# Performance work log

Measured on AMD Instinct MI355X. Metric: run time of the kernel, lower is better.

## Reference

```python
import jax, jax.numpy as jnp
import numpy as np

B, S, D, H = 4, 2048, 512, 8
HD = D // H


def rotate_half(t):
    half = t.shape[-1] // 2
    return jnp.concatenate([-t[..., half:], t[..., :half]], axis=-1)


def setup_inputs() -> dict:
    key = jax.random.key(0)
    ks = jax.random.split(key, 8)
    x = jax.random.normal(ks[0], (B, S, D), dtype=jnp.float32)
    # realistic rotary tables built from angles
    inv_freq = 1.0 / (10000.0 ** (jnp.arange(0, D // 2, dtype=jnp.float32) / (D // 2)))
    ang = jnp.arange(S, dtype=jnp.float32)[:, None] * inv_freq[None, :]  # [S, D/2]
    ang = jnp.concatenate([ang, ang], axis=-1)  # [S, D]
    cos_emb = jnp.cos(ang)[None]  # [1, S, D]
    sin_emb = jnp.sin(ang)[None]
    mask = jax.random.randint(ks[1], (B, S, S), 0, 2).astype(jnp.bool_)
    scale = 1.0 / np.sqrt(D)
    wq = jax.random.normal(ks[2], (D, D), dtype=jnp.float32) * scale
    wk = jax.random.normal(ks[3], (D, D), dtype=jnp.float32) * scale
    wv = jax.random.normal(ks[4], (D, D), dtype=jnp.float32) * scale
    wo = jax.random.normal(ks[5], (D, D), dtype=jnp.float32) * scale
    return {"x": x, "cos_emb": cos_emb, "sin_emb": sin_emb, "mask": mask,
            "wq": wq, "wk": wk, "wv": wv, "wo": wo}


def reference(x, cos_emb, sin_emb, mask, wq, wk, wv, wo):
    bsz, seqlen, dim = x.shape
    # projections (weights stored as [in, out])
    xq = x @ wq
    xk = x @ wk
    xv = x @ wv
    # RoPE applied over full dim before head split (as in original)
    xq = xq * cos_emb + rotate_half(xq) * sin_emb
    xk = xk * cos_emb + rotate_half(xk) * sin_emb
    # split heads: [B, H, S, HD]
    xq = xq.reshape(bsz, seqlen, H, HD).transpose(0, 2, 1, 3)
    xk = xk.reshape(bsz, seqlen, H, HD).transpose(0, 2, 1, 3)
    xv = xv.reshape(bsz, seqlen, H, HD).transpose(0, 2, 1, 3)
    scores = jnp.einsum('bhqd,bhkd->bhqk', xq, xk) / jnp.sqrt(jnp.float32(HD))
    scores = scores + (~mask)[:, None].astype(scores.dtype) * (-1e9)
    scores = jax.nn.softmax(scores.astype(jnp.float32), axis=-1).astype(xq.dtype)
    scores = scores * mask[:, None].astype(scores.dtype)
    out = jnp.einsum('bhqk,bhkd->bhqd', scores, xv)
    out = out.transpose(0, 2, 1, 3).reshape(bsz, seqlen, dim)
    return out @ wo
```

## Files before the change

kernel.cpp:

```cpp
#include <hip/hip_runtime.h>
#include <hip/hip_bf16.h>

typedef __bf16 bf16x8 __attribute__((ext_vector_type(8)));
typedef float f32x4 __attribute__((ext_vector_type(4)));
typedef short short8 __attribute__((ext_vector_type(8)));

#define MFMA16(a, b, c) __builtin_amdgcn_mfma_f32_16x16x32_bf16((a), (b), (c), 0, 0, 0)

static constexpr int S = 2048;
static constexpr int D = 512;
static constexpr int HD = 64;
static constexpr int KBLK = 64;
#define QSCALE 0.18033688011112042f

typedef __attribute__((address_space(1))) const unsigned int gu32;
typedef __attribute__((address_space(3))) unsigned int lu32;

__device__ __forceinline__ void gll16(const void* g, void* l) {
  __builtin_amdgcn_global_load_lds((gu32*)g, (lu32*)l, 16, 0, 0);
}

__device__ __forceinline__ unsigned short f2b(float f) {
  return __builtin_bit_cast(unsigned short, __float2bfloat16(f));
}
__device__ __forceinline__ float b2f(unsigned short u) {
  return __builtin_bit_cast(float, (unsigned)u << 16);
}

__global__ void prep_kernel(const float* __restrict__ x, unsigned short* __restrict__ xb,
                            const int* __restrict__ m, unsigned long long* __restrict__ bits,
                            const float* __restrict__ wq, const float* __restrict__ wk,
                            const float* __restrict__ wv, const float* __restrict__ wo,
                            unsigned short* __restrict__ wqkvT, unsigned short* __restrict__ woT) {
  __shared__ float t[64][65];
  const int blk = blockIdx.x;
  const int tid = threadIdx.x;
  if (blk < 4096) {
    int idx = blk * 256 + tid;
    float4 v = ((const float4*)x)[idx];
    ushort4 o;
    o.x = f2b(v.x); o.y = f2b(v.y); o.z = f2b(v.z); o.w = f2b(v.w);
    ((ushort4*)xb)[idx] = o;
  } else if (blk < 6144) {
    const int stride = 2048 * 256;
    const int lane0 = (tid & 63) == 0;
    for (int gid = (blk - 4096) * 256 + tid; gid < 4 * 2048 * 2048; gid += stride) {
      unsigned long long w = __ballot(m[gid] != 0);
      if (lane0) bits[gid >> 6] = w;
    }
  } else {
    const int tt = blk - 6144;
    const int z = tt >> 6, r = tt & 63;
    const float* w = (z == 0) ? wq : (z == 1) ? wk : (z == 2) ? wv : wo;
    unsigned short* dst = (z < 3) ? wqkvT + (size_t)z * 512 * 512 : woT;
    const int i0 = (r & 7) * 64, o0 = (r >> 3) * 64;
    for (int it = 0; it < 16; ++it) {
      int idx = it * 256 + tid;
      int ii = idx >> 6, oo = idx & 63;
      t[oo][ii] = w[(size_t)(i0 + ii) * 512 + o0 + oo];
    }
    __syncthreads();
    for (int it = 0; it < 16; ++it) {
      int idx = it * 256 + tid;
      int oo = idx >> 6, ii = idx & 63;
      int o = o0 + oo, od;
      if (z < 2) {
        const int hh = o >> 6, ff = (o >> 5) & 1, cc = o & 31;
        od = ((hh & 3) * 2 + ff) * 64 + ((hh >> 2) << 5) + cc;
      } else {
        od = o;
      }
      dst[(size_t)od * 512 + i0 + ii] = f2b(t[oo][ii]);
    }
  }
}

__global__ __launch_bounds__(256)
void gemm2(const unsigned short* __restrict__ A, const unsigned short* __restrict__ Bt,
           const float* __restrict__ cose, const float* __restrict__ sine,
           unsigned short* __restrict__ qd, unsigned short* __restrict__ kd,
           unsigned short* __restrict__ vtd) {
  __shared__ alignas(16) unsigned char smem[36864];
  unsigned short (*lds)[2][4096] = (unsigned short (*)[2][4096])smem;
  const int tid = threadIdx.x;
  const int lane = tid & 63, l15 = lane & 15, lg = lane >> 4;
  const int wave = tid >> 6;
  const int K = 512;
  const int m0 = blockIdx.x * 128, n0 = blockIdx.y * 128;
  const int wm = (wave >> 1) * 64, wn = (wave & 1) * 64;
  const int wbase = wave * 512;
  const int grow = tid >> 2, gcol = (tid & 3) * 8;
  f32x4 acc[4][4] = {};

#define GSTAGE(sb, kk)                                                              \
  do {                                                                              \
    gll16(&A[(size_t)(m0 + grow) * K + (kk) + gcol], &lds[sb][0][wbase]);           \
    gll16(&A[(size_t)(m0 + 64 + grow) * K + (kk) + gcol], &lds[sb][0][2048 + wbase]);\
    gll16(&Bt[(size_t)(n0 + grow) * K + (kk) + gcol], &lds[sb][1][wbase]);          \
    gll16(&Bt[(size_t)(n0 + 64 + grow) * K + (kk) + gcol], &lds[sb][1][2048 + wbase]);\
  } while (0)

  GSTAGE(0, 0);
  asm volatile("s_waitcnt vmcnt(0)" ::: "memory");
  __syncthreads();
  for (int t = 0; t < 16; ++t) {
    const int cur = t & 1;
    if (t + 1 < 16) GSTAGE(cur ^ 1, (t + 1) * 32);
    bf16x8 af[4], bfr[4];
#pragma unroll
    for (int i = 0; i < 4; ++i) {
      af[i]  = *(const bf16x8*)&lds[cur][0][(wm + i * 16 + l15) * 32 + lg * 8];
      bfr[i] = *(const bf16x8*)&lds[cur][1][(wn + i * 16 + l15) * 32 + lg * 8];
    }
    __builtin_amdgcn_s_setprio(1);
#pragma unroll
    for (int i = 0; i < 4; ++i)
#pragma unroll
      for (int j = 0; j < 4; ++j)
        acc[i][j] = MFMA16(af[i], bfr[j], acc[i][j]);
    __builtin_amdgcn_s_setprio(0);
    asm volatile("s_waitcnt vmcnt(0)" ::: "memory");
    __syncthreads();
  }
#undef GSTAGE

  const int sel = n0 >> 9;
  const int nb = (n0 & 511) + wn;
  const int b0 = m0 >> 11;
  if (sel < 2) {
    unsigned short* dst = (sel == 0) ? qd : kd;
    const float qs = (sel == 0) ? QSCALE : 1.f;
    const int g = nb >> 6, p = g >> 1, f = g & 1;
    const int sbase = (m0 & 2047) + wm;
#pragma unroll
    for (int i = 0; i < 4; ++i)
#pragma unroll
      for (int jl = 0; jl < 2; ++jl) {
        const int c = jl * 16 + l15;
        const int dtr = p * 64 + f * 32 + c;
        const int hd = f * 32 + c;
#pragma unroll
        for (int r = 0; r < 4; ++r) {
          const int s = sbase + i * 16 + lg * 4 + r;
          const float cs = cose[(size_t)s * 512 + dtr];
          const float sn = sine[(size_t)s * 512 + dtr];
          const float lo = acc[i][jl][r], hi = acc[i][jl + 2][r];
          dst[(((size_t)(b0 * 8) + p) * 2048 + s) * 64 + hd] = f2b((lo * cs - hi * sn) * qs);
          dst[(((size_t)(b0 * 8) + p + 4) * 2048 + s) * 64 + hd] = f2b((hi * cs + lo * sn) * qs);
        }
      }
  } else {
    unsigned short* tb = (unsigned short*)smem + wave * 4608;
#pragma unroll
    for (int i = 0; i < 4; ++i)
#pragma unroll
      for (int j = 0; j < 4; ++j) {
        ushort4 pk;
        pk.x = f2b(acc[i][j][0]); pk.y = f2b(acc[i][j][1]);
        pk.z = f2b(acc[i][j][2]); pk.w = f2b(acc[i][j][3]);
        *(ushort4*)&tb[(j * 16 + l15) * 72 + i * 16 + lg * 4] = pk;
      }
    const int s0 = (m0 & 2047) + wm;
    const int g = lane >> 3, c = lane & 7;
#pragma unroll
    for (int rr = 0; rr < 8; ++rr) {
      const int row = rr * 8 + g;
      const int nng = nb + row;
      uint4 v = *(const uint4*)&tb[row * 72 + c * 8];
      *(uint4*)&vtd[(((size_t)(b0 * 8) + (nng >> 6)) * 64 + (nng & 63)) * 2048 + s0 + c * 8] = v;
    }
  }
}

__global__ __launch_bounds__(512)
void flash_kernel(const unsigned short* __restrict__ qb, const unsigned short* __restrict__ kb,
                  const unsigned short* __restrict__ vtb, const unsigned long long* __restrict__ mbits,
                  unsigned short* __restrict__ op0, unsigned short* __restrict__ op1,
                  float* __restrict__ ls0, float* __restrict__ ls1) {
  __shared__ alignas(16) unsigned short kv[2][2][4096];
  __shared__ alignas(16) f32x4 btab[16];
  const int tid = threadIdx.x;
  const int wave = tid >> 6, lane = tid & 63;
  const int l15 = lane & 15, lg = lane >> 4;
  const int swz = (l15 & 7) << 4;
  const int wgid = blockIdx.x;
  const int slot = wgid >> 3;
  const int bh = (wgid & 7) * 4 + (slot & 3);
  const int rest = slot >> 2;
  const int kh = rest & 1;
  const int q0 = (rest >> 1) * 256 + wave * 16;
  const int b = bh >> 3, h = bh & 7;
  const int kbase = kh * 1024;
  const unsigned short* Q = qb + ((size_t)bh * S + q0) * HD;
  const unsigned short* Kp = kb + (size_t)bh * S * HD;
  const unsigned short* Vt = vtb + (size_t)bh * HD * S;
  const unsigned long long* MrowA = mbits + ((size_t)b * S + q0 + l15) * (S / 64) + kh * 16;
  const unsigned long long* MrowB = MrowA + (size_t)128 * (S / 64);
  unsigned short* opart = kh ? op1 : op0;
  float* lsum = kh ? ls1 : ls0;

  const int srow = tid >> 3;
  const int scol = ((tid & 7) ^ (srow & 7)) * 8;
  const int ksrow = ((srow & 15) >> 2) * 8 + ((srow >> 4) & 1) * 4 + (srow & 3) + (srow >> 5) * 32;
  const int wbase = wave * 512;

  if (tid < 16) {
    f32x4 e;
    e[0] = (tid & 1) ? 0.f : -300.f;
    e[1] = (tid & 2) ? 0.f : -300.f;
    e[2] = (tid & 4) ? 0.f : -300.f;
    e[3] = (tid & 8) ? 0.f : -300.f;
    btab[tid] = e;
  }

  bf16x8 qf0a = *(const bf16x8*)&Q[l15 * HD + lg * 8];
  bf16x8 qf1a = *(const bf16x8*)&Q[l15 * HD + 32 + lg * 8];
  bf16x8 qf0b = *(const bf16x8*)&Q[(128 + l15) * HD + lg * 8];
  bf16x8 qf1b = *(const bf16x8*)&Q[(128 + l15) * HD + 32 + lg * 8];
  f32x4 oa[4] = {}, ob[4] = {};
  float lpa = 0.f, lpb = 0.f;
  const int lgs8 = lg * 8;

  unsigned long long wAa = MrowA[0], wAb = MrowB[0];
  gll16(&Kp[(size_t)(kbase + ksrow) * HD + scol], &kv[0][0][wbase]);
  gll16(&Vt[(size_t)srow * S + kbase + scol], &kv[0][1][wbase]);
  asm volatile("s_waitcnt vmcnt(0) lgkmcnt(0)" ::: "memory");
  __syncthreads();

  for (int t = 0; t < 16; ++t) {
    const int cur = t & 1;
    unsigned long long wBa = 0, wBb = 0;
    if (t + 1 < 16) {
      const int kn = kbase + (t + 1) * KBLK;
      gll16(&Kp[(size_t)(kn + ksrow) * HD + scol], &kv[cur ^ 1][0][wbase]);
      gll16(&Vt[(size_t)srow * S + kn + scol], &kv[cur ^ 1][1][wbase]);
      wBa = MrowA[t + 1];
      wBb = MrowB[t + 1];
    }
    const char* kbp = (const char*)&kv[cur][0][0];
    const char* vbp = (const char*)&kv[cur][1][0];

    bf16x8 pf0a, pf1a, pf0b, pf1b;
#pragma unroll
    for (int n = 0; n < 4; ++n) {
      const int cb = (n * 16 + l15) * 128 + ((lg * 16) ^ swz);
      bf16x8 kf0 = *(const bf16x8*)(kbp + cb);
      bf16x8 kf1 = *(const bf16x8*)(kbp + (cb ^ 64));
      f32x4 scA = {}, scB = {};
      __builtin_amdgcn_s_setprio(1);
      scA = MFMA16(kf0, qf0a, scA);
      scA = MFMA16(kf1, qf1a, scA);
      scB = MFMA16(kf0, qf0b, scB);
      scB = MFMA16(kf1, qf1b, scB);
      __builtin_amdgcn_s_setprio(0);
      const int sh = (n == 0) ? 0 : (n == 1) ? 4 : (n == 2) ? 32 : 36;
      const f32x4 ba = btab[(unsigned)(wAa >> (lgs8 + sh)) & 15u];
      const f32x4 bb = btab[(unsigned)(wAb >> (lgs8 + sh)) & 15u];
      f32x4 pa, pb;
#pragma unroll
      for (int r = 0; r < 4; ++r) {
        pa[r] = __builtin_amdgcn_exp2f(scA[r] + ba[r]);
        pb[r] = __builtin_amdgcn_exp2f(scB[r] + bb[r]);
      }
      lpa += (pa[0] + pa[1]) + (pa[2] + pa[3]);
      lpb += (pb[0] + pb[1]) + (pb[2] + pb[3]);
      bf16x8& dsta = (n < 2) ? pf0a : pf1a;
      bf16x8& dstb = (n < 2) ? pf0b : pf1b;
      const int jo = (n & 1) * 4;
#pragma unroll
      for (int j = 0; j < 4; ++j) {
        dsta[jo + j] = (__bf16)pa[j];
        dstb[jo + j] = (__bf16)pb[j];
      }
    }

    __builtin_amdgcn_s_setprio(1);
#pragma unroll
    for (int n = 0; n < 4; ++n) {
      const int cb = (n * 16 + l15) * 128 + ((lg * 16) ^ swz);
      bf16x8 vf0 = *(const bf16x8*)(vbp + cb);
      bf16x8 vf1 = *(const bf16x8*)(vbp + (cb ^ 64));
      oa[n] = MFMA16(pf0a, vf0, oa[n]);
      oa[n] = MFMA16(pf1a, vf1, oa[n]);
      ob[n] = MFMA16(pf0b, vf0, ob[n]);
      ob[n] = MFMA16(pf1b, vf1, ob[n]);
    }
    __builtin_amdgcn_s_setprio(0);

    asm volatile("s_waitcnt vmcnt(0)" ::: "memory");
    __syncthreads();
    wAa = wBa;
    wAb = wBb;
  }

  lpa += __shfl_xor(lpa, 16);
  lpa += __shfl_xor(lpa, 32);
  lpb += __shfl_xor(lpb, 16);
  lpb += __shfl_xor(lpb, 32);
  if (lg == 0) {
    lsum[(size_t)bh * S + q0 + l15] = lpa;
    lsum[(size_t)bh * S + q0 + 128 + l15] = lpb;
  }
#pragma unroll
  for (int r = 0; r < 4; ++r)
#pragma unroll
    for (int n = 0; n < 4; ++n) {
      opart[((size_t)(b * S + q0 + lg * 4 + r)) * D + h * HD + n * 16 + l15] = f2b(oa[n][r]);
      opart[((size_t)(b * S + q0 + 128 + lg * 4 + r)) * D + h * HD + n * 16 + l15] = f2b(ob[n][r]);
    }
}

__global__ __launch_bounds__(256)
void gemm_fused(const unsigned short* __restrict__ op0, const unsigned short* __restrict__ op1,
                const float* __restrict__ ls0, const float* __restrict__ ls1,
                const unsigned short* __restrict__ Bt, float* __restrict__ C) {
  __shared__ alignas(16) unsigned short ldsA[2][2048];
  __shared__ alignas(16) unsigned short ldsB[2][4096];
  __shared__ float invt[512];
  const int tid = threadIdx.x;
  const int lane = tid & 63, l15 = lane & 15, lg = lane >> 4;
  const int wave = tid >> 6;
  const int m0 = blockIdx.x * 64, n0 = blockIdx.y * 128;
  const int wm = (wave >> 1) * 32, wn = (wave & 1) * 64;
  const int wbase = wave * 512;
  const int grow = tid >> 2, gcol = (tid & 3) * 8;
  const size_t abase = (size_t)(m0 + (tid >> 2)) * 512 + (tid & 3) * 8;
  f32x4 acc[2][4] = {};

  for (int e = tid; e < 512; e += 256) {
    const int row = e >> 3, hh = e & 7;
    const int m = m0 + row;
    const size_t li = ((size_t)((m >> 11) * 8 + hh)) * 2048 + (m & 2047);
    const float l = ls0[li] + ls1[li];
    invt[e] = (l > 0.f) ? 1.f / l : 0.f;
  }

#define BSTAGE(sb, kk)                                                               \
  do {                                                                               \
    gll16(&Bt[(size_t)(n0 + grow) * 512 + (kk) + gcol], &ldsB[sb][wbase]);           \
    gll16(&Bt[(size_t)(n0 + 64 + grow) * 512 + (kk) + gcol], &ldsB[sb][2048 + wbase]);\
  } while (0)

  short8 a8, p8;
#define ALOAD(kk)                                          \
  do {                                                     \
    a8 = *(const short8*)&op0[abase + (kk)];               \
    p8 = *(const short8*)&op1[abase + (kk)];               \
  } while (0)

#define AWRITE(sb, kk)                                                                   \
  do {                                                                                   \
    const float inv = invt[((tid >> 2) << 3) | ((kk) >> 6)];                             \
    short8 pk;                                                                           \
    pk[0] = (short)f2b((b2f((unsigned short)a8[0]) + b2f((unsigned short)p8[0])) * inv); \
    pk[1] = (short)f2b((b2f((unsigned short)a8[1]) + b2f((unsigned short)p8[1])) * inv); \
    pk[2] = (short)f2b((b2f((unsigned short)a8[2]) + b2f((unsigned short)p8[2])) * inv); \
    pk[3] = (short)f2b((b2f((unsigned short)a8[3]) + b2f((unsigned short)p8[3])) * inv); \
    pk[4] = (short)f2b((b2f((unsigned short)a8[4]) + b2f((unsigned short)p8[4])) * inv); \
    pk[5] = (short)f2b((b2f((unsigned short)a8[5]) + b2f((unsigned short)p8[5])) * inv); \
    pk[6] = (short)f2b((b2f((unsigned short)a8[6]) + b2f((unsigned short)p8[6])) * inv); \
    pk[7] = (short)f2b((b2f((unsigned short)a8[7]) + b2f((unsigned short)p8[7])) * inv); \
    *(short8*)&ldsA[sb][(tid >> 2) * 32 + (tid & 3) * 8] = pk;                           \
  } while (0)

  ALOAD(0);
  BSTAGE(0, 0);
  __syncthreads();
  AWRITE(0, 0);
  __syncthreads();

  for (int t = 0; t < 16; ++t) {
    const int cur = t & 1;
    const bool have = (t + 1 < 16);
    if (have) { ALOAD((t + 1) * 32); BSTAGE(cur ^ 1, (t + 1) * 32); }
    bf16x8 af[2], bfr[4];
#pragma unroll
    for (int i = 0; i < 2; ++i)
      af[i] = *(const bf16x8*)&ldsA[cur][(wm + i * 16 + l15) * 32 + lg * 8];
#pragma unroll
    for (int j = 0; j < 4; ++j)
      bfr[j] = *(const bf16x8*)&ldsB[cur][(wn + j * 16 + l15) * 32 + lg * 8];
    __builtin_amdgcn_s_setprio(1);
#pragma unroll
    for (int i = 0; i < 2; ++i)
#pragma unroll
      for (int j = 0; j < 4; ++j)
        acc[i][j] = MFMA16(af[i], bfr[j], acc[i][j]);
    __builtin_amdgcn_s_setprio(0);
    asm volatile("s_waitcnt vmcnt(0)" ::: "memory");
    __syncthreads();
    if (have) AWRITE(cur ^ 1, (t + 1) * 32);
    __syncthreads();
  }
#undef BSTAGE
#undef ALOAD
#undef AWRITE

#pragma unroll
  for (int i = 0; i < 2; ++i)
#pragma unroll
    for (int j = 0; j < 4; ++j)
#pragma unroll
      for (int r = 0; r < 4; ++r)
        C[(size_t)(m0 + wm + i * 16 + lg * 4 + r) * 512 + (n0 + wn + j * 16 + l15)] = acc[i][j][r];
}

extern "C" void kernel_launch(void* const* d_in, const int* in_sizes, int n_in,
                              void* d_out, int out_size, void* d_ws, size_t ws_size,
                              hipStream_t stream) {
  const float* x = (const float*)d_in[0];
  const float* cose = (const float*)d_in[1];
  const float* sine = (const float*)d_in[2];
  const int* mask = (const int*)d_in[3];
  const float* wq = (const float*)d_in[4];
  const float* wk = (const float*)d_in[5];
  const float* wv = (const float*)d_in[6];
  const float* wo = (const float*)d_in[7];
  float* out = (float*)d_out;
  char* ws = (char*)d_ws;

  unsigned short* xb    = (unsigned short*)(ws);
  unsigned short* wqkvT = (unsigned short*)(ws + 8388608);
  unsigned short* woT   = (unsigned short*)(ws + 9961472);
  unsigned short* qbh   = (unsigned short*)(ws + 35651584);
  unsigned short* kbh   = (unsigned short*)(ws + 44040192);
  unsigned short* vtb   = (unsigned short*)(ws + 52428800);
  unsigned long long* mbits = (unsigned long long*)(ws + 60817408);
  unsigned short* op0 = (unsigned short*)(ws + 10485760);
  unsigned short* op1 = (unsigned short*)(ws + 62914560);
  float* ls0 = (float*)(ws + 79691776);
  float* ls1 = (float*)(ws + 79953920);

  prep_kernel<<<6400, 256, 0, stream>>>(x, xb, mask, mbits, wq, wk, wv, wo, wqkvT, woT);
  gemm2<<<dim3(64, 12), 256, 0, stream>>>(xb, wqkvT, cose, sine, qbh, kbh, vtb);
  flash_kernel<<<512, 512, 0, stream>>>(qbh, kbh, vtb, mbits, op0, op1, ls0, ls1);
  gemm_fused<<<dim3(128, 4), 256, 0, stream>>>(op0, op1, ls0, ls1, woT, out);
}
```

Baseline: 107.8 us.

## Split flash attention key range into four partitions instead of two

The flash kernel now splits the key dimension four ways, using 1024 workgroups that each process 8 key blocks instead of 512 workgroups processing 16. Partial outputs and row sums go to four buffers, and the output GEMM sums all four before normalising. This targets poor latency hiding and occupancy from too few workgroups on the many CUs, at the cost of more partial-output traffic, extra loads in the final GEMM, and more prologue overhead per workgroup.

```diff
diff --git a/kernel.cpp b/kernel.cpp
--- a/kernel.cpp
+++ b/kernel.cpp
@@ -176,7 +176,9 @@
 void flash_kernel(const unsigned short* __restrict__ qb, const unsigned short* __restrict__ kb,
                   const unsigned short* __restrict__ vtb, const unsigned long long* __restrict__ mbits,
                   unsigned short* __restrict__ op0, unsigned short* __restrict__ op1,
-                  float* __restrict__ ls0, float* __restrict__ ls1) {
+                  unsigned short* __restrict__ op2, unsigned short* __restrict__ op3,
+                  float* __restrict__ ls0, float* __restrict__ ls1,
+                  float* __restrict__ ls2, float* __restrict__ ls3) {
   __shared__ alignas(16) unsigned short kv[2][2][4096];
   __shared__ alignas(16) f32x4 btab[16];
   const int tid = threadIdx.x;
@@ -187,17 +189,17 @@
   const int slot = wgid >> 3;
   const int bh = (wgid & 7) * 4 + (slot & 3);
   const int rest = slot >> 2;
-  const int kh = rest & 1;
-  const int q0 = (rest >> 1) * 256 + wave * 16;
+  const int kh = rest & 3;
+  const int q0 = (rest >> 2) * 256 + wave * 16;
   const int b = bh >> 3, h = bh & 7;
-  const int kbase = kh * 1024;
+  const int kbase = kh * 512;
   const unsigned short* Q = qb + ((size_t)bh * S + q0) * HD;
   const unsigned short* Kp = kb + (size_t)bh * S * HD;
   const unsigned short* Vt = vtb + (size_t)bh * HD * S;
-  const unsigned long long* MrowA = mbits + ((size_t)b * S + q0 + l15) * (S / 64) + kh * 16;
+  const unsigned long long* MrowA = mbits + ((size_t)b * S + q0 + l15) * (S / 64) + kh * 8;
   const unsigned long long* MrowB = MrowA + (size_t)128 * (S / 64);
-  unsigned short* opart = kh ? op1 : op0;
-  float* lsum = kh ? ls1 : ls0;
+  unsigned short* opart = (kh == 0) ? op0 : (kh == 1) ? op1 : (kh == 2) ? op2 : op3;
+  float* lsum = (kh == 0) ? ls0 : (kh == 1) ? ls1 : (kh == 2) ? ls2 : ls3;
 
   const int srow = tid >> 3;
   const int scol = ((tid & 7) ^ (srow & 7)) * 8;
@@ -227,10 +229,10 @@
   asm volatile("s_waitcnt vmcnt(0) lgkmcnt(0)" ::: "memory");
   __syncthreads();
 
-  for (int t = 0; t < 16; ++t) {
+  for (int t = 0; t < 8; ++t) {
     const int cur = t & 1;
     unsigned long long wBa = 0, wBb = 0;
-    if (t + 1 < 16) {
+    if (t + 1 < 8) {
       const int kn = kbase + (t + 1) * KBLK;
       gll16(&Kp[(size_t)(kn + ksrow) * HD + scol], &kv[cur ^ 1][0][wbase]);
       gll16(&Vt[(size_t)srow * S + kn + scol], &kv[cur ^ 1][1][wbase]);
@@ -312,7 +314,9 @@
 
 __global__ __launch_bounds__(256)
 void gemm_fused(const unsigned short* __restrict__ op0, const unsigned short* __restrict__ op1,
+                const unsigned short* __restrict__ op2, const unsigned short* __restrict__ op3,
                 const float* __restrict__ ls0, const float* __restrict__ ls1,
+                const float* __restrict__ ls2, const float* __restrict__ ls3,
                 const unsigned short* __restrict__ Bt, float* __restrict__ C) {
   __shared__ alignas(16) unsigned short ldsA[2][2048];
   __shared__ alignas(16) unsigned short ldsB[2][4096];
@@ -331,7 +335,7 @@
     const int row = e >> 3, hh = e & 7;
     const int m = m0 + row;
     const size_t li = ((size_t)((m >> 11) * 8 + hh)) * 2048 + (m & 2047);
-    const float l = ls0[li] + ls1[li];
+    const float l = ls0[li] + ls1[li] + ls2[li] + ls3[li];
     invt[e] = (l > 0.f) ? 1.f / l : 0.f;
   }
 
@@ -341,26 +345,26 @@
     gll16(&Bt[(size_t)(n0 + 64 + grow) * 512 + (kk) + gcol], &ldsB[sb][2048 + wbase]);\
   } while (0)
 
-  short8 a8, p8;
+  short8 a8, p8, c8, d8;
 #define ALOAD(kk)                                          \
   do {                                                     \
     a8 = *(const short8*)&op0[abase + (kk)];               \
     p8 = *(const short8*)&op1[abase + (kk)];               \
+    c8 = *(const short8*)&op2[abase + (kk)];               \
+    d8 = *(const short8*)&op3[abase + (kk)];               \
   } while (0)
 
-#define AWRITE(sb, kk)                                                                   \
-  do {                                                                                   \
-    const float inv = invt[((tid >> 2) << 3) | ((kk) >> 6)];                             \
-    short8 pk;                                                                           \
-    pk[0] = (short)f2b((b2f((unsigned short)a8[0]) + b2f((unsigned short)p8[0])) * inv); \
-    pk[1] = (short)f2b((b2f((unsigned short)a8[1]) + b2f((unsigned short)p8[1])) * inv); \
-    pk[2] = (short)f2b((b2f((unsigned short)a8[2]) + b2f((unsigned short)p8[2])) * inv); \
-    pk[3] = (short)f2b((b2f((unsigned short)a8[3]) + b2f((unsigned short)p8[3])) * inv); \
-    pk[4] = (short)f2b((b2f((unsigned short)a8[4]) + b2f((unsigned short)p8[4])) * inv); \
-    pk[5] = (short)f2b((b2f((unsigned short)a8[5]) + b2f((unsigned short)p8[5])) * inv); \
-    pk[6] = (short)f2b((b2f((unsigned short)a8[6]) + b2f((unsigned short)p8[6])) * inv); \
-    pk[7] = (short)f2b((b2f((unsigned short)a8[7]) + b2f((unsigned short)p8[7])) * inv); \
-    *(short8*)&ldsA[sb][(tid >> 2) * 32 + (tid & 3) * 8] = pk;                           \
+#define AWRITE(sb, kk)                                                        \
+  do {                                                                        \
+    const float inv = invt[((tid >> 2) << 3) | ((kk) >> 6)];                  \
+    short8 pk;                                                                \
+    _Pragma("unroll")                                                         \
+    for (int e = 0; e < 8; ++e) {                                             \
+      const float s = (b2f((unsigned short)a8[e]) + b2f((unsigned short)p8[e])) + \
+                      (b2f((unsigned short)c8[e]) + b2f((unsigned short)d8[e]));  \
+      pk[e] = (short)f2b(s * inv);                                            \
+    }                                                                         \
+    *(short8*)&ldsA[sb][(tid >> 2) * 32 + (tid & 3) * 8] = pk;                \
   } while (0)
 
   ALOAD(0);
@@ -422,17 +426,22 @@
   unsigned short* xb    = (unsigned short*)(ws);
   unsigned short* wqkvT = (unsigned short*)(ws + 8388608);
   unsigned short* woT   = (unsigned short*)(ws + 9961472);
+  unsigned short* op0   = (unsigned short*)(ws + 10485760);
+  unsigned short* op1   = (unsigned short*)(ws + 18874368);
+  unsigned short* op2   = (unsigned short*)(ws + 27262976);
   unsigned short* qbh   = (unsigned short*)(ws + 35651584);
   unsigned short* kbh   = (unsigned short*)(ws + 44040192);
   unsigned short* vtb   = (unsigned short*)(ws + 52428800);
   unsigned long long* mbits = (unsigned long long*)(ws + 60817408);
-  unsigned short* op0 = (unsigned short*)(ws + 10485760);
-  unsigned short* op1 = (unsigned short*)(ws + 62914560);
-  float* ls0 = (float*)(ws + 79691776);
-  float* ls1 = (float*)(ws + 79953920);
+  unsigned short* op3   = (unsigned short*)(ws + 62914560);
+  float* ls0 = (float*)(ws + 71303168);
+  float* ls1 = (float*)(ws + 71565312);
+  float* ls2 = (float*)(ws + 71827456);
+  float* ls3 = (float*)(ws + 72089600);
 
   prep_kernel<<<6400, 256, 0, stream>>>(x, xb, mask, mbits, wq, wk, wv, wo, wqkvT, woT);
   gemm2<<<dim3(64, 12), 256, 0, stream>>>(xb, wqkvT, cose, sine, qbh, kbh, vtb);
-  flash_kernel<<<512, 512, 0, stream>>>(qbh, kbh, vtb, mbits, op0, op1, ls0, ls1);
-  gemm_fused<<<dim3(128, 4), 256, 0, stream>>>(op0, op1, ls0, ls1, woT, out);
-}
+  flash_kernel<<<1024, 512, 0, stream>>>(qbh, kbh, vtb, mbits, op0, op1, op2, op3,
+                                         ls0, ls1, ls2, ls3);
+  gemm_fused<<<dim3(128, 4), 256, 0, stream>>>(op0, op1, op2, op3, ls0, ls1, ls2, ls3, woT, out);
+}
```

Result: slower. 116.7 us (+8.2%).
